# Kernel tuning notes

Hardware: AMD Instinct MI355X
Metric: run time of the kernel (lower is better)

The kernel has to match this reference:

```python
import jax, jax.numpy as jnp
from jax import lax
import numpy as np


def setup_inputs() -> dict:
    key = jax.random.key(0)
    encode_image = jax.random.normal(key, (32, 3, 512, 512), dtype=jnp.float32)
    return {"encode_image": encode_image, "w": 5}


def _box_blur(x, w):
    # cv2.blur with ksize (w, w): normalized box filter, BORDER_REFLECT_101 padding.
    # Implemented as a separable depthwise convolution (two 1D average passes).
    B, C, H, W = x.shape
    p = w // 2  # w is odd -> symmetric padding, matches cv2 default anchor
    xp = jnp.pad(x, ((0, 0), (0, 0), (p, p), (p, p)), mode="reflect")  # REFLECT_101
    kh = jnp.full((C, 1, w, 1), 1.0 / w, dtype=x.dtype)  # vertical pass
    kw = jnp.full((C, 1, 1, w), 1.0 / w, dtype=x.dtype)  # horizontal pass
    dn = ("NCHW", "OIHW", "NCHW")
    y = lax.conv_general_dilated(xp, kh, (1, 1), "VALID",
                                 dimension_numbers=dn, feature_group_count=C)
    y = lax.conv_general_dilated(y, kw, (1, 1), "VALID",
                                 dimension_numbers=dn, feature_group_count=C)
    return y  # (B, C, H, W)


def reference(encode_image, w):
    # Faithful to Smooth.forward: replaces noise_and_cover[0] with the box-blurred
    # image; we return the blurred tensor (the only modified element).
    return _box_blur(encode_image, w)
```

## Files before the change

kernel.cpp:

```cpp
#include <hip/hip_runtime.h>


#define TILE 64
#define HALO 2
#define TIN  (TILE + 2 * HALO)
#define PADI (TIN + 1)

__global__ __launch_bounds__(256) void smooth_box5_kernel(
    const float* __restrict__ in, float* __restrict__ out, int H, int W)
{
    __shared__ float s_in[TIN][PADI];
    __shared__ float s_h [TIN][TILE];

    const int tid   = threadIdx.x;
    const int tileX = blockIdx.x * TILE;
    const int tileY = blockIdx.y * TILE;
    const long long plane = blockIdx.z;

    const float* __restrict__ ip = in  + plane * (long long)H * W;
    float*       __restrict__ op = out + plane * (long long)H * W;

    #pragma unroll 4
    for (int i = tid; i < TIN * TIN; i += 256) {
        int r = i / TIN;
        int c = i - r * TIN;
        int gy = tileY + r - HALO;
        int gx = tileX + c - HALO;
        gy = (gy < 0) ? -gy : ((gy >= H) ? (2 * H - 2 - gy) : gy);
        gx = (gx < 0) ? -gx : ((gx >= W) ? (2 * W - 2 - gx) : gx);
        s_in[r][c] = ip[(long long)gy * W + gx];
    }
    __syncthreads();

    #pragma unroll 4
    for (int i = tid; i < TIN * TILE; i += 256) {
        int r = i >> 6;
        int c = i & (TILE - 1);
        float v = s_in[r][c] + s_in[r][c + 1] + s_in[r][c + 2]
                + s_in[r][c + 3] + s_in[r][c + 4];
        s_h[r][c] = v * 0.2f;
    }
    __syncthreads();

    #pragma unroll 4
    for (int i = tid; i < TILE * TILE; i += 256) {
        int r = i >> 6;
        int c = i & (TILE - 1);
        float v = s_h[r][c] + s_h[r + 1][c] + s_h[r + 2][c]
                + s_h[r + 3][c] + s_h[r + 4][c];
        op[(long long)(tileY + r) * W + (tileX + c)] = v * 0.2f;
    }
}

extern "C" void kernel_launch(void* const* d_in, const int* in_sizes, int n_in,
                              void* d_out, int out_size, void* d_ws, size_t ws_size,
                              hipStream_t stream) {
    const float* img = (const float*)d_in[0];
    float* out = (float*)d_out;
    const int B = 32, C = 3, H = 512, W = 512;
    dim3 grid(W / TILE, H / TILE, B * C);
    dim3 block(256);
    smooth_box5_kernel<<<grid, block, 0, stream>>>(img, out, H, W);
}
```

Before: 193.0 us.

## Replace shared-memory tiled box blur with register sliding-window float4 kernel

The shared-memory two-pass tile kernel is replaced by a register-only design. Each thread owns four columns and 16 consecutive rows, computes horizontal sums from float4/float2 global loads, and keeps a running vertical sum over a 5-row ring buffer. This removes LDS traffic, the barriers and the redundant halo loads, and vectorizes stores. In exchange it relies on overlapping neighbor loads hitting the L1/L2 cache, and the sliding add/subtract changes the float rounding order.

Measured after the change: 197.7 us. 2.4% more time.

```diff
diff --git a/kernel.cpp b/kernel.cpp
--- a/kernel.cpp
+++ b/kernel.cpp
@@ -1,54 +1,75 @@
 #include <hip/hip_runtime.h>
 
 
-#define TILE 64
-#define HALO 2
-#define TIN  (TILE + 2 * HALO)
-#define PADI (TIN + 1)
+#define WID 512
+#define HEI 512
+#define RPT 16
+#define TXN 16
+#define TYN 16
+
+__device__ __forceinline__ float4 add4(float4 a, float4 b) {
+    return make_float4(a.x + b.x, a.y + b.y, a.z + b.z, a.w + b.w);
+}
+__device__ __forceinline__ float4 sub4(float4 a, float4 b) {
+    return make_float4(a.x - b.x, a.y - b.y, a.z - b.z, a.w - b.w);
+}
 
 __global__ __launch_bounds__(256) void smooth_box5_kernel(
-    const float* __restrict__ in, float* __restrict__ out, int H, int W)
+    const float* __restrict__ in, float* __restrict__ out)
 {
-    __shared__ float s_in[TIN][PADI];
-    __shared__ float s_h [TIN][TILE];
-
-    const int tid   = threadIdx.x;
-    const int tileX = blockIdx.x * TILE;
-    const int tileY = blockIdx.y * TILE;
+    const int tid = threadIdx.x;
+    const int tx  = tid & (TXN - 1);
+    const int ty  = tid >> 4;
+    const int c   = blockIdx.x * (TXN * 4) + tx * 4;
+    const int r0  = blockIdx.y * (TYN * RPT) + ty * RPT;
     const long long plane = blockIdx.z;
 
-    const float* __restrict__ ip = in  + plane * (long long)H * W;
-    float*       __restrict__ op = out + plane * (long long)H * W;
+    const float* __restrict__ ip = in  + plane * (long long)(HEI * WID);
+    float*       __restrict__ op = out + plane * (long long)(HEI * WID);
 
-    #pragma unroll 4
-    for (int i = tid; i < TIN * TIN; i += 256) {
-        int r = i / TIN;
-        int c = i - r * TIN;
-        int gy = tileY + r - HALO;
-        int gx = tileX + c - HALO;
-        gy = (gy < 0) ? -gy : ((gy >= H) ? (2 * H - 2 - gy) : gy);
-        gx = (gx < 0) ? -gx : ((gx >= W) ? (2 * W - 2 - gx) : gx);
-        s_in[r][c] = ip[(long long)gy * W + gx];
-    }
-    __syncthreads();
+    const bool leftE  = (c == 0);
+    const bool rightE = (c == WID - 4);
 
-    #pragma unroll 4
-    for (int i = tid; i < TIN * TILE; i += 256) {
-        int r = i >> 6;
-        int c = i & (TILE - 1);
-        float v = s_in[r][c] + s_in[r][c + 1] + s_in[r][c + 2]
-                + s_in[r][c + 3] + s_in[r][c + 4];
-        s_h[r][c] = v * 0.2f;
-    }
-    __syncthreads();
+    auto hsum = [&](int gy) -> float4 {
+        gy = (gy < 0) ? -gy : ((gy >= HEI) ? (2 * HEI - 2 - gy) : gy);
+        const float* row = ip + gy * WID;
+        float4 m = *reinterpret_cast<const float4*>(row + c);
+        float2 l, r;
+        if (leftE)  l = make_float2(m.z, m.y);
+        else        l = *reinterpret_cast<const float2*>(row + c - 2);
+        if (rightE) r = make_float2(m.z, m.y);
+        else        r = *reinterpret_cast<const float2*>(row + c + 4);
+        float t  = m.y + m.z;
+        float u  = m.x + t;
+        float v  = t + m.w;
+        float s4 = u + m.w;
+        float4 h;
+        h.x = (l.x + l.y) + u;
+        h.y = l.y + s4;
+        h.z = s4 + r.x;
+        h.w = v + (r.x + r.y);
+        return h;
+    };
 
-    #pragma unroll 4
-    for (int i = tid; i < TILE * TILE; i += 256) {
-        int r = i >> 6;
-        int c = i & (TILE - 1);
-        float v = s_h[r][c] + s_h[r + 1][c] + s_h[r + 2][c]
-                + s_h[r + 3][c] + s_h[r + 4][c];
-        op[(long long)(tileY + r) * W + (tileX + c)] = v * 0.2f;
+    float4 h[5];
+    h[0] = hsum(r0 - 2);
+    h[1] = hsum(r0 - 1);
+    h[2] = hsum(r0);
+    h[3] = hsum(r0 + 1);
+    float4 vs = add4(add4(h[0], h[1]), add4(h[2], h[3]));
+
+    float* orow = op + r0 * WID + c;
+
+    #pragma unroll
+    for (int k = 0; k < RPT; ++k) {
+        float4 hn = hsum(r0 + 2 + k);
+        h[(4 + k) % 5] = hn;
+        vs = add4(vs, hn);
+        float4 o = make_float4(vs.x * 0.04f, vs.y * 0.04f,
+                               vs.z * 0.04f, vs.w * 0.04f);
+        *reinterpret_cast<float4*>(orow) = o;
+        vs = sub4(vs, h[k % 5]);
+        orow += WID;
     }
 }
 
@@ -57,8 +78,8 @@
                               hipStream_t stream) {
     const float* img = (const float*)d_in[0];
     float* out = (float*)d_out;
-    const int B = 32, C = 3, H = 512, W = 512;
-    dim3 grid(W / TILE, H / TILE, B * C);
+    const int B = 32, C = 3;
+    dim3 grid(WID / (TXN * 4), HEI / (TYN * RPT), B * C);
     dim3 block(256);
-    smooth_box5_kernel<<<grid, block, 0, stream>>>(img, out, H, W);
+    smooth_box5_kernel<<<grid, block, 0, stream>>>(img, out);
 }
```
